# Kernel tuning notes

Measured on AMD Instinct MI355X. Metric: run time of the kernel, lower is better.

The kernel has to match this reference:

```python
import jax, jax.numpy as jnp
import numpy as np

D = 384
K = 16
RADII = (1.0, 2.0, 4.0, 8.0)


def layer_norm(x, g, b, eps=1e-5):
    m = jnp.mean(x, axis=-1, keepdims=True)
    v = jnp.var(x, axis=-1, keepdims=True)
    return (x - m) * jax.lax.rsqrt(v + eps) * g + b


def fps(pos, M):
    # Farthest point sampling: deterministic start at index 0. pos: (N,3) -> (M,) int indices.
    dmin0 = jnp.sum((pos - pos[0]) ** 2, axis=-1)

    def step(dmin, _):
        nxt = jnp.argmax(dmin)
        d = jnp.sum((pos - pos[nxt]) ** 2, axis=-1)
        return jnp.minimum(dmin, d), nxt

    _, rest = jax.lax.scan(step, dmin0, None, length=M - 1)
    return jnp.concatenate([jnp.zeros((1,), rest.dtype), rest])


def sa_stage(x, pos, r, lw, lb, sw, dw, pw1, pb1, pw2, pb2, aw, ab, lg, lbt):
    # One set-abstraction stage for a single point cloud. x:(N,D), pos:(N,3).
    N = x.shape[0]
    M = N // 4  # ratio = 0.25
    idx = fps(pos, M)
    q_pos = pos[idx]  # (M,3)
    # k-nearest neighbors within radius r (radius grouping)
    d2 = jnp.sum((q_pos[:, None, :] - pos[None, :, :]) ** 2, axis=-1)  # (M,N)
    neg_d, nbr = jax.lax.top_k(-d2, K)  # (M,K) nearest sources
    valid = (-neg_d) <= r * r  # (M,K); self point (dist 0) always valid
    # PointTransformerConv
    v = x @ lw + lb        # lin (value path)
    a_src = x @ sw         # lin_src, no bias
    a_dst = x[idx] @ dw    # lin_dst, no bias
    rel = q_pos[:, None, :] - pos[nbr]  # (M,K,3)  pos_i - pos_j
    delta = jax.nn.relu(jax.nn.relu(rel @ pw1 + pb1) @ pw2 + pb2)  # pos_nn, (M,K,D)
    alpha = jax.nn.relu((a_dst[:, None, :] - a_src[nbr] + delta) @ aw + ab)  # attn_nn
    alpha = jnp.where(valid[:, :, None], alpha, -1e30)
    attn = jax.nn.softmax(alpha, axis=1) * valid[:, :, None]  # per-dst, per-channel softmax
    out = jnp.sum(attn * (v[nbr] + delta), axis=1)  # (M,D) weighted aggregation
    return layer_norm(out, lg, lbt), q_pos


def setup_inputs() -> dict:
    key = jax.random.key(0)
    ks = jax.random.split(key, 8)
    B, N = 4, 4096
    s = 0.05
    inp = {"pts": jax.random.normal(ks[0], (B, N, 3 + D), jnp.float32)}
    inp["lin_w"] = jax.random.normal(ks[1], (4, D, D), jnp.float32) * s
    inp["lin_b"] = jnp.zeros((4, D), jnp.float32)
    inp["src_w"] = jax.random.normal(ks[2], (4, D, D), jnp.float32) * s
    inp["dst_w"] = jax.random.normal(ks[3], (4, D, D), jnp.float32) * s
    inp["pos_w1"] = jax.random.normal(ks[4], (4, 3, D), jnp.float32) * s
    inp["pos_b1"] = jnp.zeros((4, D), jnp.float32)
    inp["pos_w2"] = jax.random.normal(ks[5], (4, D, D), jnp.float32) * s
    inp["pos_b2"] = jnp.zeros((4, D), jnp.float32)
    inp["attn_w"] = jax.random.normal(ks[6], (4, D, D), jnp.float32) * s
    inp["attn_b"] = jnp.zeros((4, D), jnp.float32)
    inp["ln_g"] = jnp.ones((4, D), jnp.float32)
    inp["ln_b"] = jnp.zeros((4, D), jnp.float32)
    inp["proj_w"] = jax.random.normal(ks[7], (D, D), jnp.float32) * s
    inp["proj_b"] = jnp.zeros((D,), jnp.float32)
    inp["pln_g"] = jnp.ones((D,), jnp.float32)
    inp["pln_b"] = jnp.zeros((D,), jnp.float32)
    return inp


def reference(pts, lin_w, lin_b, src_w, dst_w, pos_w1, pos_b1, pos_w2, pos_b2,
              attn_w, attn_b, ln_g, ln_b, proj_w, proj_b, pln_g, pln_b):
    pos = pts[..., :3]
    x = pts[..., 3:]  # in_proj is Identity (in_dim == out_dim)
    for s in range(4):
        stage_fn = lambda xx, pp, s=s: sa_stage(
            xx, pp, RADII[s], lin_w[s], lin_b[s], src_w[s], dst_w[s],
            pos_w1[s], pos_b1[s], pos_w2[s], pos_b2[s], attn_w[s], attn_b[s],
            ln_g[s], ln_b[s])
        x, pos = jax.vmap(stage_fn)(x, pos)
    feat = layer_norm(x @ proj_w + proj_b, pln_g, pln_b)
    pad = jnp.zeros(feat.shape[:2], dtype=bool)  # ~pad_mask: all points valid
    return pos, feat, pad
```

## Files before the change

kernel.cpp:

```cpp
#include <hip/hip_runtime.h>
#include <math.h>


using half8 = __attribute__((ext_vector_type(8))) _Float16;
using f32x4 = __attribute__((ext_vector_type(4))) float;

__device__ __forceinline__ float d2f(float ax, float ay, float az,
                                     float bx, float by, float bz)
{
  const float dx = __fsub_rn(ax, bx);
  const float dy = __fsub_rn(ay, by);
  const float dz = __fsub_rn(az, bz);
  return __fadd_rn(__fadd_rn(__fmul_rn(dx, dx), __fmul_rn(dy, dy)),
                   __fmul_rn(dz, dz));
}

template<int CTRL>
__device__ __forceinline__ unsigned dppmax_step(unsigned v)
{
  const unsigned o = (unsigned)__builtin_amdgcn_update_dpp(
      (int)v, (int)v, CTRL, 0xF, 0xF, false);
  return o > v ? o : v;
}
__device__ __forceinline__ unsigned wave_max_bcast(unsigned v)
{
  v = dppmax_step<0x111>(v);
  v = dppmax_step<0x112>(v);
  v = dppmax_step<0x114>(v);
  v = dppmax_step<0x118>(v);
  v = dppmax_step<0x142>(v);
  v = dppmax_step<0x143>(v);
  return (unsigned)__builtin_amdgcn_readlane((int)v, 63);
}

__global__ __launch_bounds__(128) void split_kernel(
    const float* __restrict__ pts, float* __restrict__ pos0, float* __restrict__ x0)
{
  const int n = blockIdx.x;
  const int b = blockIdx.y;
  const float* src = pts + ((long)b * 4096 + n) * 387;
  float* pd = pos0 + ((long)b * 4096 + n) * 3;
  float* xd = x0 + ((long)b * 4096 + n) * 384;
  for (int e = threadIdx.x; e < 387; e += 128) {
    float v = src[e];
    if (e < 3) pd[e] = v; else xd[e - 3] = v;
  }
}

struct TP { const float* src[5]; _Float16* dst; };
__global__ __launch_bounds__(256) void transpose_kernel(TP p)
{
  const int z = blockIdx.z;
  const float* S = p.src[z >> 2] + (long)(z & 3) * 147456;
  _Float16* Dst = p.dst + (long)z * 147456;
  const int k0 = blockIdx.x * 32, n0 = blockIdx.y * 32;
  __shared__ float tile[32][33];
  const int ti = threadIdx.x & 31, tj = threadIdx.x >> 5;
  #pragma unroll
  for (int p8 = 0; p8 < 32; p8 += 8)
    tile[tj + p8][ti] = S[(long)(k0 + tj + p8) * 384 + n0 + ti];
  __syncthreads();
  #pragma unroll
  for (int p8 = 0; p8 < 32; p8 += 8)
    Dst[(long)(n0 + tj + p8) * 384 + k0 + ti] = (_Float16)tile[ti][tj + p8];
}

template<int NPTS, int NTHR>
__device__ __forceinline__ void fps_body(
    const float* __restrict__ pos,
    int* __restrict__ idx_out, float* __restrict__ pos_out,
    int b, int t,
    float* __restrict__ spx, float* __restrict__ spy, float* __restrict__ spz,
    unsigned long long* __restrict__ s_key)
{
  constexpr int NPT = NPTS / NTHR;
  constexpr int NW = NTHR / 64;
  constexpr int M = NPTS / 4;
  pos += (long)b * NPTS * 3; idx_out += (long)b * M; pos_out += (long)b * M * 3;

  float px[NPT], py[NPT], pz[NPT], dmin[NPT];
  #pragma unroll
  for (int i = 0; i < NPT; i++) {
    const int j = t * NPT + i;
    px[i] = pos[j*3]; py[i] = pos[j*3+1]; pz[i] = pos[j*3+2];
    spx[j] = px[i]; spy[j] = py[i]; spz[j] = pz[i];
  }
  const float sx = pos[0], sy = pos[1], sz = pos[2];
  float bv = 0.f; int bi = 0;
  #pragma unroll
  for (int i = 0; i < NPT; i++) {
    const float dd = d2f(px[i], py[i], pz[i], sx, sy, sz);
    dmin[i] = dd;
    if (i == 0) { bv = dd; bi = 0; }
    else { const bool g = dd > bv; bv = g ? dd : bv; bi = g ? i : bi; }
  }
  if (t == 0) { idx_out[0] = 0; pos_out[0] = sx; pos_out[1] = sy; pos_out[2] = sz; }
  if (NW > 1) __syncthreads();

  for (int m = 1; m < M; ++m) {
    const unsigned myub = __float_as_uint(bv);
    const unsigned wmax = wave_max_bcast(myub);
    const unsigned long long mk = __ballot(myub == wmax);
    const int srclane = __builtin_ctzll(mk);
    const int lbi = __shfl(bi, srclane);
    const int wj = ((t & ~63) + srclane) * NPT + lbi;

    int sel;
    if (NW > 1) {
      const int p = m & 1;
      if ((t & 63) == 0)
        s_key[p*NW + (t >> 6)] =
            ((unsigned long long)wmax << 32) | (unsigned)(NPTS - 1 - wj);
      __syncthreads();
      unsigned long long kb = s_key[p*NW];
      #pragma unroll
      for (int w2 = 1; w2 < NW; w2++) {
        const unsigned long long o = s_key[p*NW + w2];
        if (o > kb) kb = o;
      }
      sel = NPTS - 1 - (int)(kb & 0xFFFFFFFFu);
    } else {
      sel = wj;
    }
    const float qx = spx[sel], qy = spy[sel], qz = spz[sel];
    if (t == 0) { idx_out[m] = sel; pos_out[m*3] = qx; pos_out[m*3+1] = qy; pos_out[m*3+2] = qz; }
    float nbv = 0.f; int nbi = 0;
    #pragma unroll
    for (int i = 0; i < NPT; i++) {
      const float dd = d2f(px[i], py[i], pz[i], qx, qy, qz);
      const float nd = fminf(dmin[i], dd);
      dmin[i] = nd;
      if (i == 0) { nbv = nd; nbi = 0; }
      else { const bool g = nd > nbv; nbv = g ? nd : nbv; nbi = g ? i : nbi; }
    }
    bv = nbv; bi = nbi;
  }
}

template<int NPTS, int NTHR>
__global__ __launch_bounds__(NTHR, 1) void fps_kernel(
    const float* __restrict__ pos,
    int* __restrict__ idx_out, float* __restrict__ pos_out)
{
  __shared__ float spx[NPTS], spy[NPTS], spz[NPTS];
  __shared__ unsigned long long s_key[2 * (NTHR > 64 ? NTHR / 64 : 1)];
  fps_body<NPTS, NTHR>(pos, idx_out, pos_out, blockIdx.x, threadIdx.x,
                       spx, spy, spz, s_key);
}

template<int C>
__global__ __launch_bounds__(64) void knn_kernel(
    const float* __restrict__ pos, const float* __restrict__ qpos,
    int N, int M, int* __restrict__ nbr, float* __restrict__ vld, float r2)
{
  const int m = blockIdx.x, b = blockIdx.y;
  pos += (long)b * N * 3; qpos += (long)b * M * 3;
  nbr += (long)b * (1024 * 16); vld += (long)b * (1024 * 16);
  const int lane = threadIdx.x;
  const float qx = qpos[m*3], qy = qpos[m*3+1], qz = qpos[m*3+2];
  unsigned long long key[C];
  #pragma unroll
  for (int c = 0; c < C; c++) {
    const int j = c * 64 + lane;
    const float dd = d2f(pos[j*3], pos[j*3+1], pos[j*3+2], qx, qy, qz);
    key[c] = ((unsigned long long)__float_as_uint(dd) << 32) | (unsigned)j;
  }
  unsigned long long prev = 0;
  for (int k = 0; k < 16; k++) {
    unsigned long long best = ~0ull;
    #pragma unroll
    for (int c = 0; c < C; c++) {
      const bool take = (k == 0) || (key[c] > prev);
      if (take && key[c] < best) best = key[c];
    }
    #pragma unroll
    for (int off = 32; off; off >>= 1) {
      const unsigned long long o = __shfl_xor(best, off);
      if (o < best) best = o;
    }
    prev = best;
    if (lane == 0) {
      nbr[m*16+k] = (int)(best & 0xFFFFFFFFu);
      const float dd = __uint_as_float((unsigned)(best >> 32));
      vld[m*16+k] = (dd <= r2) ? 1.0f : 0.0f;
    }
  }
}

struct GemmP {
  const float* A; long sA;
  const _Float16* Wt;
  const float* bias;
  float* C; long sC;
  int R;
  const int* gather; long sG;
  const float* qpos; long sQ;
  const float* pos;  long sP;
  const int* nbr;    long sN;
  const float* pw1;
  const float* pb1;
  const float* adst; long sAD;
  const float* asrc; long sAS;
  int row0;
};

typedef _Float16 (*H40)[40];

template<int AMODE, bool GATHER, bool BIAS, bool RELU>
__device__ __forceinline__ void mgemm_body(
    const GemmP& p, int bx, int by, int bz, int t, H40 As, H40 Bs)
{
  const int b = bz;
  const int rb = bx * 64;
  const int cb = by * 64;
  const float* A = p.A ? (p.A + (long)b * p.sA) : nullptr;
  float* C = p.C + (long)b * p.sC;
  const int* gat = GATHER ? (p.gather + (long)b * p.sG) : nullptr;
  const int* nbrb = (AMODE != 0) ? (p.nbr + (long)b * p.sN) : nullptr;

  const int w = t >> 6, lane = t & 63;
  const int wm = w & 1, wn = w >> 1;
  const int quad = lane >> 4, l16 = lane & 15;

  f32x4 acc[2][2] = {};

  const int sr = t >> 2;
  const int sk = (t & 3) << 3;
  const int ar = rb + sr;

  const float* arow = nullptr;
  const float* adrow = nullptr;
  const float* asrow = nullptr;
  bool avalid = true;
  float rx = 0.f, ry = 0.f, rz = 0.f;
  if (AMODE == 0) {
    avalid = (ar < p.R);
    long srcrow = 0;
    if (avalid) srcrow = GATHER ? (long)gat[ar] : (long)ar;
    arow = A + srcrow * 384;
  } else {
    const int grow = p.row0 + ar;
    const int mq = grow >> 4;
    const int n = nbrb[grow];
    if (AMODE == 1) {
      const float* qposb = p.qpos + (long)b * p.sQ;
      const float* posb = p.pos + (long)b * p.sP;
      rx = qposb[mq*3+0] - posb[n*3+0];
      ry = qposb[mq*3+1] - posb[n*3+1];
      rz = qposb[mq*3+2] - posb[n*3+2];
    } else {
      arow = A + (long)ar * 384;
      adrow = p.adst + (long)b * p.sAD + (long)mq * 384;
      asrow = p.asrc + (long)b * p.sAS + (long)n * 384;
    }
  }

  for (int k0 = 0; k0 < 384; k0 += 32) {
    float a8[8];
    if (AMODE == 0) {
      if (avalid) {
        const float4 u = *(const float4*)(arow + k0 + sk);
        const float4 v = *(const float4*)(arow + k0 + sk + 4);
        a8[0]=u.x; a8[1]=u.y; a8[2]=u.z; a8[3]=u.w;
        a8[4]=v.x; a8[5]=v.y; a8[6]=v.z; a8[7]=v.w;
      } else {
        #pragma unroll
        for (int j = 0; j < 8; j++) a8[j] = 0.f;
      }
    } else if (AMODE == 1) {
      const int kc = k0 + sk;
      const float4 w0a = *(const float4*)(p.pw1 + kc);
      const float4 w0b = *(const float4*)(p.pw1 + kc + 4);
      const float4 w1a = *(const float4*)(p.pw1 + 384 + kc);
      const float4 w1b = *(const float4*)(p.pw1 + 384 + kc + 4);
      const float4 w2a = *(const float4*)(p.pw1 + 768 + kc);
      const float4 w2b = *(const float4*)(p.pw1 + 768 + kc + 4);
      const float4 b1a = *(const float4*)(p.pb1 + kc);
      const float4 b1b = *(const float4*)(p.pb1 + kc + 4);
      a8[0] = fmaxf(rx*w0a.x + ry*w1a.x + rz*w2a.x + b1a.x, 0.f);
      a8[1] = fmaxf(rx*w0a.y + ry*w1a.y + rz*w2a.y + b1a.y, 0.f);
      a8[2] = fmaxf(rx*w0a.z + ry*w1a.z + rz*w2a.z + b1a.z, 0.f);
      a8[3] = fmaxf(rx*w0a.w + ry*w1a.w + rz*w2a.w + b1a.w, 0.f);
      a8[4] = fmaxf(rx*w0b.x + ry*w1b.x + rz*w2b.x + b1b.x, 0.f);
      a8[5] = fmaxf(rx*w0b.y + ry*w1b.y + rz*w2b.y + b1b.y, 0.f);
      a8[6] = fmaxf(rx*w0b.z + ry*w1b.z + rz*w2b.z + b1b.z, 0.f);
      a8[7] = fmaxf(rx*w0b.w + ry*w1b.w + rz*w2b.w + b1b.w, 0.f);
    } else {
      const int kc = k0 + sk;
      const float4 d0 = *(const float4*)(arow + kc);
      const float4 d1 = *(const float4*)(arow + kc + 4);
      const float4 a0 = *(const float4*)(adrow + kc);
      const float4 a1 = *(const float4*)(adrow + kc + 4);
      const float4 s0 = *(const float4*)(asrow + kc);
      const float4 s1 = *(const float4*)(asrow + kc + 4);
      a8[0] = a0.x - s0.x + d0.x; a8[1] = a0.y - s0.y + d0.y;
      a8[2] = a0.z - s0.z + d0.z; a8[3] = a0.w - s0.w + d0.w;
      a8[4] = a1.x - s1.x + d1.x; a8[5] = a1.y - s1.y + d1.y;
      a8[6] = a1.z - s1.z + d1.z; a8[7] = a1.w - s1.w + d1.w;
    }
    const half8 bv = *(const half8*)(p.Wt + (long)(cb + sr) * 384 + k0 + sk);

    __syncthreads();
    half8 av;
    #pragma unroll
    for (int j = 0; j < 8; j++) av[j] = (_Float16)a8[j];
    *(half8*)&As[sr][sk] = av;
    *(half8*)&Bs[sr][sk] = bv;
    __syncthreads();

    const half8 fa0 = *(const half8*)&As[wm*32 + l16][quad*8];
    const half8 fa1 = *(const half8*)&As[wm*32 + 16 + l16][quad*8];
    const half8 fb0 = *(const half8*)&Bs[wn*32 + l16][quad*8];
    const half8 fb1 = *(const half8*)&Bs[wn*32 + 16 + l16][quad*8];
    acc[0][0] = __builtin_amdgcn_mfma_f32_16x16x32_f16(fa0, fb0, acc[0][0], 0, 0, 0);
    acc[0][1] = __builtin_amdgcn_mfma_f32_16x16x32_f16(fa0, fb1, acc[0][1], 0, 0, 0);
    acc[1][0] = __builtin_amdgcn_mfma_f32_16x16x32_f16(fa1, fb0, acc[1][0], 0, 0, 0);
    acc[1][1] = __builtin_amdgcn_mfma_f32_16x16x32_f16(fa1, fb1, acc[1][1], 0, 0, 0);
  }

  float bi0 = 0.f, bi1 = 0.f;
  if (BIAS) {
    bi0 = p.bias[cb + wn*32 + l16];
    bi1 = p.bias[cb + wn*32 + 16 + l16];
  }
  #pragma unroll
  for (int i = 0; i < 2; i++) {
    const int base = rb + wm*32 + i*16;
    if (base < p.R) {
      const int r0 = base + quad*4;
      #pragma unroll
      for (int j = 0; j < 2; j++) {
        const int col = cb + wn*32 + j*16 + l16;
        const float bb = j ? bi1 : bi0;
        #pragma unroll
        for (int reg = 0; reg < 4; reg++) {
          float v = acc[i][j][reg] + bb;
          if (RELU) v = fmaxf(v, 0.f);
          C[(long)(r0 + reg) * 384 + col] = v;
        }
      }
    }
  }
}

template<int AMODE, bool GATHER, bool BIAS, bool RELU>
__global__ __launch_bounds__(256) void mgemm_kernel(GemmP p)
{
  __shared__ _Float16 As[64][40];
  __shared__ _Float16 Bs[64][40];
  mgemm_body<AMODE, GATHER, BIAS, RELU>(p, blockIdx.x, blockIdx.y, blockIdx.z,
                                        threadIdx.x, As, Bs);
}

__global__ __launch_bounds__(256) void fat1_kernel(
    const float* fpos, int* fidx, float* fpout, GemmP gv, GemmP ga)
{
  __shared__ char buf[49664] __attribute__((aligned(16)));
  int bid = blockIdx.x; const int t = threadIdx.x;
  if (bid < 4) {
    float* spx = (float*)buf;
    float* spy = spx + 4096;
    float* spz = spy + 4096;
    unsigned long long* s_key = (unsigned long long*)(spz + 4096);
    fps_body<4096, 256>(fpos, fidx, fpout, bid, t, spx, spy, spz, s_key);
    return;
  }
  bid -= 4;
  H40 As = (H40)buf;
  H40 Bs = (H40)(buf + 64 * 40 * sizeof(_Float16));
  if (bid < 1536) {
    mgemm_body<0, false, true, false>(gv, bid & 63, (bid >> 6) % 6, bid / 384, t, As, Bs);
    return;
  }
  bid -= 1536;
  mgemm_body<0, false, false, false>(ga, bid & 63, (bid >> 6) % 6, bid / 384, t, As, Bs);
}

__global__ __launch_bounds__(128) void attnln_kernel(
    const float* __restrict__ alpha, const float* __restrict__ delta,
    const float* __restrict__ vbuf, const int* __restrict__ nbr,
    const float* __restrict__ vldb, const float* __restrict__ lng,
    const float* __restrict__ lnb, float* __restrict__ xout,
    int q0, long sCh, long sV, long sNb, long sX)
{
  const int ml = blockIdx.x, b = blockIdx.y;
  const int m = q0 + ml;
  alpha += (long)b * sCh; delta += (long)b * sCh; vbuf += (long)b * sV;
  nbr += (long)b * sNb; vldb += (long)b * sNb; xout += (long)b * sX;
  const int t = threadIdx.x;

  int nb[16]; float vl[16];
  #pragma unroll
  for (int k = 0; k < 16; k++) { nb[k] = nbr[m*16+k]; vl[k] = vldb[m*16+k]; }

  const long rbase = (long)ml * 16 * 384;
  float av[16][3];
  #pragma unroll
  for (int k = 0; k < 16; k++)
    #pragma unroll
    for (int i = 0; i < 3; i++) {
      const float a = alpha[rbase + k*384 + t + i*128];
      av[k][i] = (vl[k] > 0.5f) ? a : -1e30f;
    }
  float mx[3] = {-3.4e38f, -3.4e38f, -3.4e38f};
  #pragma unroll
  for (int k = 0; k < 16; k++)
    #pragma unroll
    for (int i = 0; i < 3; i++) mx[i] = fmaxf(mx[i], av[k][i]);
  float sm[3] = {0.f, 0.f, 0.f};
  #pragma unroll
  for (int k = 0; k < 16; k++)
    #pragma unroll
    for (int i = 0; i < 3; i++) { const float e = expf(av[k][i] - mx[i]); av[k][i] = e; sm[i] += e; }
  float rs[3];
  #pragma unroll
  for (int i = 0; i < 3; i++) rs[i] = 1.0f / sm[i];
  float o[3] = {0.f, 0.f, 0.f};
  #pragma unroll
  for (int k = 0; k < 16; k++) {
    const long nrow = (long)nb[k] * 384;
    #pragma unroll
    for (int i = 0; i < 3; i++) {
      const int dd = t + i * 128;
      const float vv = vbuf[nrow + dd] + delta[rbase + k*384 + dd];
      o[i] += (av[k][i] * rs[i] * vl[k]) * vv;
    }
  }
  __shared__ float sred[2];
  float s1 = o[0] + o[1] + o[2];
  #pragma unroll
  for (int off = 32; off; off >>= 1) s1 += __shfl_xor(s1, off);
  if ((t & 63) == 0) sred[t >> 6] = s1;
  __syncthreads();
  const float mean = (sred[0] + sred[1]) * (1.0f / 384.0f);
  __syncthreads();
  float s2 = 0.f;
  #pragma unroll
  for (int i = 0; i < 3; i++) { const float dd = o[i] - mean; s2 += dd * dd; }
  #pragma unroll
  for (int off = 32; off; off >>= 1) s2 += __shfl_xor(s2, off);
  if ((t & 63) == 0) sred[t >> 6] = s2;
  __syncthreads();
  const float var = (sred[0] + sred[1]) * (1.0f / 384.0f);
  const float rstd = 1.0f / sqrtf(var + 1e-5f);
  #pragma unroll
  for (int i = 0; i < 3; i++) {
    const int dd = t + i * 128;
    xout[(long)m * 384 + dd] = (o[i] - mean) * rstd * lng[dd] + lnb[dd];
  }
}

__global__ __launch_bounds__(384) void feat_kernel(
    const float* __restrict__ x4, const float* __restrict__ pw,
    const float* __restrict__ pb, const float* __restrict__ g,
    const float* __restrict__ be, float* __restrict__ outf)
{
  const int row = blockIdx.x, b = blockIdx.y;
  const long r = (long)b * 16 + row;
  const int d = threadIdx.x;
  __shared__ float xs[384];
  xs[d] = x4[r * 384 + d];
  __syncthreads();
  float acc = pb[d];
  #pragma unroll 8
  for (int j = 0; j < 384; j++) acc = fmaf(xs[j], pw[(long)j * 384 + d], acc);
  __shared__ float sred[6];
  float s = acc;
  #pragma unroll
  for (int off = 32; off; off >>= 1) s += __shfl_xor(s, off);
  if ((d & 63) == 0) sred[d >> 6] = s;
  __syncthreads();
  const float mean = (sred[0]+sred[1]+sred[2]+sred[3]+sred[4]+sred[5]) * (1.0f/384.0f);
  __syncthreads();
  float dv = (acc - mean) * (acc - mean);
  #pragma unroll
  for (int off = 32; off; off >>= 1) dv += __shfl_xor(dv, off);
  if ((d & 63) == 0) sred[d >> 6] = dv;
  __syncthreads();
  const float var = (sred[0]+sred[1]+sred[2]+sred[3]+sred[4]+sred[5]) * (1.0f/384.0f);
  const float rstd = 1.0f / sqrtf(var + 1e-5f);
  outf[r * 384 + d] = (acc - mean) * rstd * g[d] + be[d];
}

__global__ void tail_kernel(const float* __restrict__ p4, float* __restrict__ out)
{
  const int t = threadIdx.x;
  if (t < 192) out[t] = p4[t];
  if (t < 64) out[192 + 24576 + t] = 0.0f;
}

extern "C" void kernel_launch(void* const* d_in, const int* in_sizes, int n_in,
                              void* d_out, int out_size, void* d_ws, size_t ws_size,
                              hipStream_t stream)
{
  (void)in_sizes; (void)n_in; (void)out_size; (void)ws_size;
  const float* pts    = (const float*)d_in[0];
  const float* lin_w  = (const float*)d_in[1];
  const float* lin_b  = (const float*)d_in[2];
  const float* src_w  = (const float*)d_in[3];
  const float* dst_w  = (const float*)d_in[4];
  const float* pos_w1 = (const float*)d_in[5];
  const float* pos_b1 = (const float*)d_in[6];
  const float* pos_w2 = (const float*)d_in[7];
  const float* pos_b2 = (const float*)d_in[8];
  const float* attn_w = (const float*)d_in[9];
  const float* attn_b = (const float*)d_in[10];
  const float* ln_g   = (const float*)d_in[11];
  const float* ln_b   = (const float*)d_in[12];
  const float* proj_w = (const float*)d_in[13];
  const float* proj_b = (const float*)d_in[14];
  const float* pln_g  = (const float*)d_in[15];
  const float* pln_b  = (const float*)d_in[16];
  float* out = (float*)d_out;

  constexpr long SX0 = 4096L*384, SX1 = 1024L*384, SX2 = 256L*384, SX3 = 64L*384, SX4 = 16L*384;
  constexpr long SP0 = 4096L*3, SP1 = 1024L*3, SP2 = 256L*3, SP3 = 64L*3, SP4 = 16L*3;
  constexpr long SV  = 4096L*384;
  constexpr long SAD = 1024L*384;
  constexpr long SCH = 4096L*384;
  constexpr long SNB = 1024L*16;

  _Float16* wt = (_Float16*)d_ws;
  float* ws = (float*)(wt + 20L * 147456);
  float* x0 = ws; ws += 4*SX0;
  float* x1 = ws; ws += 4*SX1;
  float* x2 = ws; ws += 4*SX2;
  float* x3 = ws; ws += 4*SX3;
  float* x4 = ws; ws += 4*SX4;
  float* p0 = ws; ws += 4*SP0;
  float* p1 = ws; ws += 4*SP1;
  float* p2 = ws; ws += 4*SP2;
  float* p3 = ws; ws += 4*SP3;
  float* p4 = ws; ws += 4*SP4;
  float* vb = ws; ws += 4*SV;
  float* asb = ws; ws += 4*SV;
  float* adb = ws; ws += 4*SAD;
  float* db = ws; ws += 4*SCH;
  float* ab = ws; ws += 4*SCH;
  float* vld = ws; ws += 4*SNB;
  int* nb = (int*)ws; ws += 4*SNB;
  int* ix[4];
  ix[0] = (int*)ws; ws += 4*1024;
  ix[1] = (int*)ws; ws += 4*256;
  ix[2] = (int*)ws; ws += 4*64;
  ix[3] = (int*)ws; ws += 4*16;

  const int Ns[4] = {4096, 1024, 256, 64};
  const int Ms[4] = {1024, 256, 64, 16};
  const float R2[4] = {1.0f, 4.0f, 16.0f, 64.0f};
  float* X[5] = {x0, x1, x2, x3, x4};
  float* P[5] = {p0, p1, p2, p3, p4};
  long SPs[5] = {SP0, SP1, SP2, SP3, SP4};
  long SXs[5] = {SX0, SX1, SX2, SX3, SX4};

  split_kernel<<<dim3(4096, 4), 128, 0, stream>>>(pts, p0, x0);

  {
    TP tp{};
    tp.src[0] = lin_w; tp.src[1] = src_w; tp.src[2] = dst_w;
    tp.src[3] = pos_w2; tp.src[4] = attn_w;
    tp.dst = wt;
    transpose_kernel<<<dim3(12, 12, 20), 256, 0, stream>>>(tp);
  }

  {
    GemmP gv{}; gv.A = x0; gv.sA = SX0; gv.Wt = wt + (long)(0*4+0)*147456;
    gv.bias = lin_b; gv.C = vb; gv.sC = SV; gv.R = 4096;
    GemmP ga{}; ga.A = x0; ga.sA = SX0; ga.Wt = wt + (long)(1*4+0)*147456;
    ga.C = asb; ga.sC = SV; ga.R = 4096;
    fat1_kernel<<<dim3(4 + 1536 + 1536), 256, 0, stream>>>(p0, ix[0], p1, gv, ga);
  }

  fps_kernel<1024, 256><<<dim3(4), 256, 0, stream>>>(P[1], ix[1], P[2]);
  fps_kernel<256, 64><<<dim3(4), 64, 0, stream>>>(P[2], ix[2], P[3]);
  fps_kernel<64, 64><<<dim3(4), 64, 0, stream>>>(P[3], ix[3], P[4]);

  for (int s = 0; s < 4; s++) {
    const int N = Ns[s], M = Ms[s];
    switch (s) {
      case 0: knn_kernel<64><<<dim3(M, 4), 64, 0, stream>>>(P[s], P[s+1], N, M, nb, vld, R2[s]); break;
      case 1: knn_kernel<16><<<dim3(M, 4), 64, 0, stream>>>(P[s], P[s+1], N, M, nb, vld, R2[s]); break;
      case 2: knn_kernel<4><<<dim3(M, 4), 64, 0, stream>>>(P[s], P[s+1], N, M, nb, vld, R2[s]); break;
      default: knn_kernel<1><<<dim3(M, 4), 64, 0, stream>>>(P[s], P[s+1], N, M, nb, vld, R2[s]); break;
    }
    if (s > 0) {
      GemmP g{}; g.A = X[s]; g.sA = SXs[s]; g.Wt = wt + (long)(0*4+s)*147456; g.bias = lin_b + (long)s*384;
      g.C = vb; g.sC = SV; g.R = N;
      mgemm_kernel<0, false, true, false><<<dim3(N/64, 6, 4), 256, 0, stream>>>(g);
      GemmP g2{}; g2.A = X[s]; g2.sA = SXs[s]; g2.Wt = wt + (long)(1*4+s)*147456;
      g2.C = asb; g2.sC = SV; g2.R = N;
      mgemm_kernel<0, false, false, false><<<dim3(N/64, 6, 4), 256, 0, stream>>>(g2);
    }
    {
      GemmP g{}; g.A = X[s]; g.sA = SXs[s]; g.Wt = wt + (long)(2*4+s)*147456;
      g.C = adb; g.sC = SAD; g.R = M; g.gather = ix[s]; g.sG = M;
      mgemm_kernel<0, true, false, false><<<dim3((M+63)/64, 6, 4), 256, 0, stream>>>(g);
    }
    const int nch = (M + 255) / 256;
    for (int c = 0; c < nch; c++) {
      const int q0 = c * 256;
      const int Mc = (M - q0 < 256) ? (M - q0) : 256;
      const int rows = Mc * 16;
      {
        GemmP g{}; g.Wt = wt + (long)(3*4+s)*147456; g.bias = pos_b2 + (long)s*384;
        g.C = db; g.sC = SCH; g.R = rows;
        g.qpos = P[s+1]; g.sQ = SPs[s+1]; g.pos = P[s]; g.sP = SPs[s];
        g.nbr = nb; g.sN = SNB; g.pw1 = pos_w1 + (long)s*1152; g.pb1 = pos_b1 + (long)s*384;
        g.row0 = q0 * 16;
        mgemm_kernel<1, false, true, true><<<dim3(rows/64, 6, 4), 256, 0, stream>>>(g);
      }
      {
        GemmP g{}; g.A = db; g.sA = SCH; g.Wt = wt + (long)(4*4+s)*147456; g.bias = attn_b + (long)s*384;
        g.C = ab; g.sC = SCH; g.R = rows;
        g.nbr = nb; g.sN = SNB; g.adst = adb; g.sAD = SAD; g.asrc = asb; g.sAS = SV;
        g.row0 = q0 * 16;
        mgemm_kernel<2, false, true, true><<<dim3(rows/64, 6, 4), 256, 0, stream>>>(g);
      }
      attnln_kernel<<<dim3(Mc, 4), 128, 0, stream>>>(
          ab, db, vb, nb, vld, ln_g + (long)s*384, ln_b + (long)s*384,
          X[s+1], q0, SCH, SV, SNB, (long)M*384);
    }
  }

  feat_kernel<<<dim3(16, 4), 384, 0, stream>>>(x4, proj_w, proj_b, pln_g, pln_b, out + 192);
  tail_kernel<<<1, 256, 0, stream>>>(p4, out);
}
```

Measured before the change: 1.458 ms.

## Fuse FPS, kNN and dst-GEMM into combined launches with FPS wave priority

Adds fat2_kernel, which runs stage-1 FPS, stage-0 kNN (four queries per 256-thread block) and the stage-0 gathered dst GEMM in one launch. For stages 1-3, sfat_kernel merges the value, src and dst GEMMs with kNN into a single launch. It also raises wave priority for the serial FPS blocks so they keep pace alongside the co-resident GEMM work. The goal is to cut launch count and overlap the long serial FPS with parallel work, at the cost of larger shared-memory footprints and mixed block types competing for CUs.

```diff
diff --git a/kernel.cpp b/kernel.cpp
--- a/kernel.cpp
+++ b/kernel.cpp
@@ -4,6 +4,13 @@
 
 using half8 = __attribute__((ext_vector_type(8))) _Float16;
 using f32x4 = __attribute__((ext_vector_type(4))) float;
+
+__device__ __forceinline__ void fps_prio()
+{
+#if __has_builtin(__builtin_amdgcn_s_setprio)
+  __builtin_amdgcn_s_setprio(3);
+#endif
+}
 
 __device__ __forceinline__ float d2f(float ax, float ay, float az,
                                      float bx, float by, float bz)
@@ -149,14 +156,13 @@
 }
 
 template<int C>
-__global__ __launch_bounds__(64) void knn_kernel(
-    const float* __restrict__ pos, const float* __restrict__ qpos,
-    int N, int M, int* __restrict__ nbr, float* __restrict__ vld, float r2)
-{
-  const int m = blockIdx.x, b = blockIdx.y;
-  pos += (long)b * N * 3; qpos += (long)b * M * 3;
+__device__ __forceinline__ void knn_body(
+    const float* __restrict__ pos, const float* __restrict__ qpos, int M,
+    int* __restrict__ nbr, float* __restrict__ vld, float r2,
+    int b, int m, int lane)
+{
+  pos += (long)b * (C * 64) * 3; qpos += (long)b * M * 3;
   nbr += (long)b * (1024 * 16); vld += (long)b * (1024 * 16);
-  const int lane = threadIdx.x;
   const float qx = qpos[m*3], qy = qpos[m*3+1], qz = qpos[m*3+2];
   unsigned long long key[C];
   #pragma unroll
@@ -185,6 +191,15 @@
       vld[m*16+k] = (dd <= r2) ? 1.0f : 0.0f;
     }
   }
+}
+
+template<int C>
+__global__ __launch_bounds__(64) void knn_kernel(
+    const float* __restrict__ pos, const float* __restrict__ qpos,
+    int N, int M, int* __restrict__ nbr, float* __restrict__ vld, float r2)
+{
+  (void)N;
+  knn_body<C>(pos, qpos, M, nbr, vld, r2, blockIdx.y, blockIdx.x, threadIdx.x);
 }
 
 struct GemmP {
@@ -358,6 +373,7 @@
   __shared__ char buf[49664] __attribute__((aligned(16)));
   int bid = blockIdx.x; const int t = threadIdx.x;
   if (bid < 4) {
+    fps_prio();
     float* spx = (float*)buf;
     float* spy = spx + 4096;
     float* spz = spy + 4096;
@@ -374,6 +390,67 @@
   }
   bid -= 1536;
   mgemm_body<0, false, false, false>(ga, bid & 63, (bid >> 6) % 6, bid / 384, t, As, Bs);
+}
+
+__global__ __launch_bounds__(256) void fat2_kernel(
+    const float* fpos, int* fidx, float* fpout,
+    const float* kpos, const float* kqpos, int* knbr, float* kvld, float kr2,
+    GemmP gd)
+{
+  __shared__ char buf[12352] __attribute__((aligned(16)));
+  int bid = blockIdx.x; const int t = threadIdx.x;
+  if (bid < 4) {
+    fps_prio();
+    float* spx = (float*)buf;
+    float* spy = spx + 1024;
+    float* spz = spy + 1024;
+    unsigned long long* s_key = (unsigned long long*)(spz + 1024);
+    fps_body<1024, 256>(fpos, fidx, fpout, bid, t, spx, spy, spz, s_key);
+    return;
+  }
+  bid -= 4;
+  if (bid < 1024) {
+    const int b = bid >> 8;
+    const int q = (bid & 255) * 4 + (t >> 6);
+    knn_body<64>(kpos, kqpos, 1024, knbr, kvld, kr2, b, q, t & 63);
+    return;
+  }
+  bid -= 1024;
+  H40 As = (H40)buf;
+  H40 Bs = (H40)(buf + 64 * 40 * sizeof(_Float16));
+  mgemm_body<0, true, false, false>(gd, bid & 15, (bid >> 4) % 6, bid / 96, t, As, Bs);
+}
+
+template<int C>
+__global__ __launch_bounds__(256) void sfat_kernel(
+    GemmP gv, GemmP ga, GemmP gd,
+    const float* kpos, const float* kqpos, int kM,
+    int* knbr, float* kvld, float kr2,
+    int nv, int gxv, int nk, int gxd)
+{
+  __shared__ char buf[10240] __attribute__((aligned(16)));
+  int bid = blockIdx.x; const int t = threadIdx.x;
+  H40 As = (H40)buf;
+  H40 Bs = (H40)(buf + 64 * 40 * sizeof(_Float16));
+  if (bid < nv) {
+    mgemm_body<0, false, true, false>(gv, bid % gxv, (bid / gxv) % 6, bid / (gxv * 6), t, As, Bs);
+    return;
+  }
+  bid -= nv;
+  if (bid < nv) {
+    mgemm_body<0, false, false, false>(ga, bid % gxv, (bid / gxv) % 6, bid / (gxv * 6), t, As, Bs);
+    return;
+  }
+  bid -= nv;
+  if (bid < nk) {
+    const int qpb = kM >> 2;
+    const int b = bid / qpb;
+    const int q = (bid % qpb) * 4 + (t >> 6);
+    knn_body<C>(kpos, kqpos, kM, knbr, kvld, kr2, b, q, t & 63);
+    return;
+  }
+  bid -= nk;
+  mgemm_body<0, true, false, false>(gd, bid % gxd, (bid / gxd) % 6, bid / (gxd * 6), t, As, Bs);
 }
 
 __global__ __launch_bounds__(128) void attnln_kernel(
@@ -571,55 +648,79 @@
     fat1_kernel<<<dim3(4 + 1536 + 1536), 256, 0, stream>>>(p0, ix[0], p1, gv, ga);
   }
 
-  fps_kernel<1024, 256><<<dim3(4), 256, 0, stream>>>(P[1], ix[1], P[2]);
+  {
+    GemmP gd{}; gd.A = x0; gd.sA = SX0; gd.Wt = wt + (long)(2*4+0)*147456;
+    gd.C = adb; gd.sC = SAD; gd.R = 1024; gd.gather = ix[0]; gd.sG = 1024;
+    fat2_kernel<<<dim3(4 + 1024 + 384), 256, 0, stream>>>(
+        p1, ix[1], p2, p0, p1, nb, vld, R2[0], gd);
+  }
+
   fps_kernel<256, 64><<<dim3(4), 64, 0, stream>>>(P[2], ix[2], P[3]);
   fps_kernel<64, 64><<<dim3(4), 64, 0, stream>>>(P[3], ix[3], P[4]);
 
-  for (int s = 0; s < 4; s++) {
+  for (int c = 0; c < 4; c++) {
+    const int q0 = c * 256;
+    const int rows = 256 * 16;
+    {
+      GemmP g{}; g.Wt = wt + (long)(3*4+0)*147456; g.bias = pos_b2;
+      g.C = db; g.sC = SCH; g.R = rows;
+      g.qpos = p1; g.sQ = SP1; g.pos = p0; g.sP = SP0;
+      g.nbr = nb; g.sN = SNB; g.pw1 = pos_w1; g.pb1 = pos_b1;
+      g.row0 = q0 * 16;
+      mgemm_kernel<1, false, true, true><<<dim3(rows/64, 6, 4), 256, 0, stream>>>(g);
+    }
+    {
+      GemmP g{}; g.A = db; g.sA = SCH; g.Wt = wt + (long)(4*4+0)*147456; g.bias = attn_b;
+      g.C = ab; g.sC = SCH; g.R = rows;
+      g.nbr = nb; g.sN = SNB; g.adst = adb; g.sAD = SAD; g.asrc = asb; g.sAS = SV;
+      g.row0 = q0 * 16;
+      mgemm_kernel<2, false, true, true><<<dim3(rows/64, 6, 4), 256, 0, stream>>>(g);
+    }
+    attnln_kernel<<<dim3(256, 4), 128, 0, stream>>>(
+        ab, db, vb, nb, vld, ln_g, ln_b, x1, q0, SCH, SV, SNB, 1024L*384);
+  }
+
+  for (int s = 1; s < 4; s++) {
     const int N = Ns[s], M = Ms[s];
-    switch (s) {
-      case 0: knn_kernel<64><<<dim3(M, 4), 64, 0, stream>>>(P[s], P[s+1], N, M, nb, vld, R2[s]); break;
-      case 1: knn_kernel<16><<<dim3(M, 4), 64, 0, stream>>>(P[s], P[s+1], N, M, nb, vld, R2[s]); break;
-      case 2: knn_kernel<4><<<dim3(M, 4), 64, 0, stream>>>(P[s], P[s+1], N, M, nb, vld, R2[s]); break;
-      default: knn_kernel<1><<<dim3(M, 4), 64, 0, stream>>>(P[s], P[s+1], N, M, nb, vld, R2[s]); break;
-    }
-    if (s > 0) {
-      GemmP g{}; g.A = X[s]; g.sA = SXs[s]; g.Wt = wt + (long)(0*4+s)*147456; g.bias = lin_b + (long)s*384;
-      g.C = vb; g.sC = SV; g.R = N;
-      mgemm_kernel<0, false, true, false><<<dim3(N/64, 6, 4), 256, 0, stream>>>(g);
-      GemmP g2{}; g2.A = X[s]; g2.sA = SXs[s]; g2.Wt = wt + (long)(1*4+s)*147456;
-      g2.C = asb; g2.sC = SV; g2.R = N;
-      mgemm_kernel<0, false, false, false><<<dim3(N/64, 6, 4), 256, 0, stream>>>(g2);
-    }
+    const int gxv = N / 64, gxd = (M + 63) / 64;
+    const int nv = gxv * 24, nk = M, nd = gxd * 24;
     {
-      GemmP g{}; g.A = X[s]; g.sA = SXs[s]; g.Wt = wt + (long)(2*4+s)*147456;
-      g.C = adb; g.sC = SAD; g.R = M; g.gather = ix[s]; g.sG = M;
-      mgemm_kernel<0, true, false, false><<<dim3((M+63)/64, 6, 4), 256, 0, stream>>>(g);
-    }
-    const int nch = (M + 255) / 256;
-    for (int c = 0; c < nch; c++) {
-      const int q0 = c * 256;
-      const int Mc = (M - q0 < 256) ? (M - q0) : 256;
-      const int rows = Mc * 16;
-      {
-        GemmP g{}; g.Wt = wt + (long)(3*4+s)*147456; g.bias = pos_b2 + (long)s*384;
-        g.C = db; g.sC = SCH; g.R = rows;
-        g.qpos = P[s+1]; g.sQ = SPs[s+1]; g.pos = P[s]; g.sP = SPs[s];
-        g.nbr = nb; g.sN = SNB; g.pw1 = pos_w1 + (long)s*1152; g.pb1 = pos_b1 + (long)s*384;
-        g.row0 = q0 * 16;
-        mgemm_kernel<1, false, true, true><<<dim3(rows/64, 6, 4), 256, 0, stream>>>(g);
+      GemmP gv{}; gv.A = X[s]; gv.sA = SXs[s]; gv.Wt = wt + (long)(0*4+s)*147456;
+      gv.bias = lin_b + (long)s*384; gv.C = vb; gv.sC = SV; gv.R = N;
+      GemmP ga{}; ga.A = X[s]; ga.sA = SXs[s]; ga.Wt = wt + (long)(1*4+s)*147456;
+      ga.C = asb; ga.sC = SV; ga.R = N;
+      GemmP gd{}; gd.A = X[s]; gd.sA = SXs[s]; gd.Wt = wt + (long)(2*4+s)*147456;
+      gd.C = adb; gd.sC = SAD; gd.R = M; gd.gather = ix[s]; gd.sG = M;
+      const int total = nv + nv + nk + nd;
+      switch (s) {
+        case 1: sfat_kernel<16><<<dim3(total), 256, 0, stream>>>(
+            gv, ga, gd, P[s], P[s+1], M, nb, vld, R2[s], nv, gxv, nk, gxd); break;
+        case 2: sfat_kernel<4><<<dim3(total), 256, 0, stream>>>(
+            gv, ga, gd, P[s], P[s+1], M, nb, vld, R2[s], nv, gxv, nk, gxd); break;
+        default: sfat_kernel<1><<<dim3(total), 256, 0, stream>>>(
+            gv, ga, gd, P[s], P[s+1], M, nb, vld, R2[s], nv, gxv, nk, gxd); break;
       }
-      {
-        GemmP g{}; g.A = db; g.sA = SCH; g.Wt = wt + (long)(4*4+s)*147456; g.bias = attn_b + (long)s*384;
-        g.C = ab; g.sC = SCH; g.R = rows;
-        g.nbr = nb; g.sN = SNB; g.adst = adb; g.sAD = SAD; g.asrc = asb; g.sAS = SV;
-        g.row0 = q0 * 16;
-        mgemm_kernel<2, false, true, true><<<dim3(rows/64, 6, 4), 256, 0, stream>>>(g);
-      }
-      attnln_kernel<<<dim3(Mc, 4), 128, 0, stream>>>(
-          ab, db, vb, nb, vld, ln_g + (long)s*384, ln_b + (long)s*384,
-          X[s+1], q0, SCH, SV, SNB, (long)M*384);
-    }
+    }
+    const int rows = M * 16;
+    const int gx = rows / 64;
+    {
+      GemmP g{}; g.Wt = wt + (long)(3*4+s)*147456; g.bias = pos_b2 + (long)s*384;
+      g.C = db; g.sC = SCH; g.R = rows;
+      g.qpos = P[s+1]; g.sQ = SPs[s+1]; g.pos = P[s]; g.sP = SPs[s];
+      g.nbr = nb; g.sN = SNB; g.pw1 = pos_w1 + (long)s*1152; g.pb1 = pos_b1 + (long)s*384;
+      g.row0 = 0;
+      mgemm_kernel<1, false, true, true><<<dim3(gx, 6, 4), 256, 0, stream>>>(g);
+    }
+    {
+      GemmP g{}; g.A = db; g.sA = SCH; g.Wt = wt + (long)(4*4+s)*147456;
+      g.bias = attn_b + (long)s*384; g.C = ab; g.sC = SCH; g.R = rows;
+      g.nbr = nb; g.sN = SNB; g.adst = adb; g.sAD = SAD; g.asrc = asb; g.sAS = SV;
+      g.row0 = 0;
+      mgemm_kernel<2, false, true, true><<<dim3(gx, 6, 4), 256, 0, stream>>>(g);
+    }
+    attnln_kernel<<<dim3(M, 4), 128, 0, stream>>>(
+        ab, db, vb, nb, vld, ln_g + (long)s*384, ln_b + (long)s*384,
+        X[s+1], 0, SCH, SV, SNB, (long)M*384);
   }
 
   feat_kernel<<<dim3(16, 4), 384, 0, stream>>>(x4, proj_w, proj_b, pln_g, pln_b, out + 192);
```

After: 1.331 ms. 8.7% less time.
